# Kernel tuning notes

Hardware: AMD Instinct MI355X
Metric: run time of the kernel (lower is better)

Reference implementation:

```python
import jax, jax.numpy as jnp
import numpy as np

SEQ, B, NIN, NHID = 512, 64, 1024, 1024

def setup_inputs() -> dict:
    key = jax.random.key(0)
    k1, k2, k3 = jax.random.split(key, 3)
    x = jax.random.normal(k1, (SEQ, B, NIN), dtype=jnp.float32)
    # nn.Linear(ninput+nhid, 4*nhid): weight (4*nhid, ninput+nhid), bias (4*nhid,)
    bound = 1.0 / np.sqrt(NIN + NHID)
    W = jax.random.uniform(k2, (4 * NHID, NIN + NHID), dtype=jnp.float32, minval=-bound, maxval=bound)
    b = jax.random.uniform(k3, (4 * NHID,), dtype=jnp.float32, minval=-bound, maxval=bound)
    return {"x": x, "W": W, "b": b}

def reference(x, W, b):
    nhid = W.shape[0] // 4
    batch = x.shape[1]
    # split weight: columns [0:NIN] act on x_t, [NIN:] act on h
    def step(carry, x_t):
        h, c = carry
        a = jnp.concatenate([x_t, h], axis=1) @ W.T + b  # (B, 4*nhid)
        i = jax.nn.sigmoid(a[:, :nhid])
        f = jax.nn.sigmoid(a[:, nhid:2 * nhid])
        o = jax.nn.sigmoid(a[:, 2 * nhid:3 * nhid])
        g = jnp.tanh(a[:, 3 * nhid:])
        c = c * f + i * g
        h = o * jnp.tanh(c)
        return (h, c), h
    h0 = jnp.zeros((batch, nhid), dtype=x.dtype)
    c0 = jnp.zeros((batch, nhid), dtype=x.dtype)
    (h, c), output = jax.lax.scan(step, (h0, c0), x)
    return (output, h)
```

## Files before the change

kernel.cpp:

```cpp
#include <hip/hip_runtime.h>
#include <hip/hip_bf16.h>
#include <stdint.h>
#include <stddef.h>

#define SEQ   512
#define BATCH 64
#define NIN   1024
#define NHID  1024
#define NG    4096

typedef __attribute__((ext_vector_type(8))) short bf16x8;
typedef __attribute__((ext_vector_type(4))) float f32x4;
typedef __attribute__((ext_vector_type(4))) uint32_t u32x4;

static __device__ __forceinline__ ushort f2bf(float f) {
  uint32_t u = __builtin_bit_cast(uint32_t, f);
  uint32_t lsb = (u >> 16) & 1u;
  u += 0x7fffu + lsb;
  return (ushort)(u >> 16);
}
static __device__ __forceinline__ ushort f2h(float f) {
  _Float16 h = (_Float16)f;
  return __builtin_bit_cast(ushort, h);
}
static __device__ __forceinline__ float h2f(ushort u) {
  return (float)__builtin_bit_cast(_Float16, u);
}

static __device__ __forceinline__ f32x4 mfma_bf16(bf16x8 a, bf16x8 b, f32x4 c) {
  return __builtin_amdgcn_mfma_f32_16x16x32_bf16(a, b, c, 0, 0, 0);
}

static __device__ __forceinline__ void lds_load16(const ushort* g, ushort* l) {
  __builtin_amdgcn_global_load_lds(
      (const __attribute__((address_space(1))) void*)g,
      (__attribute__((address_space(3))) void*)l, 16, 0, 0);
}

static __device__ __forceinline__ void st_short_dev(ushort* p, uint32_t v) {
  asm volatile("global_store_short %0, %1, off sc1" :: "v"(p), "v"(v) : "memory");
}
static __device__ __forceinline__ void st_dword_dev(uint32_t* p, uint32_t v) {
  asm volatile("global_store_dword %0, %1, off sc1" :: "v"(p), "v"(v) : "memory");
}
static __device__ __forceinline__ void st_x4_dev(ushort* p, u32x4 v) {
  asm volatile("global_store_dwordx4 %0, %1, off sc1" :: "v"(p), "v"(v) : "memory");
}
static __device__ __forceinline__ uint32_t ld_dword_dev(const uint32_t* p) {
  uint32_t v;
  asm volatile("global_load_dword %0, %1, off sc1" : "=v"(v) : "v"(p) : "memory");
  return v;
}
static __device__ __forceinline__ u32x4 ld_x4_dev(const ushort* p) {
  u32x4 v;
  asm volatile("global_load_dwordx4 %0, %1, off sc1" : "=v"(v) : "v"(p) : "memory");
  return v;
}

#define WAITV(n) do { asm volatile("s_waitcnt vmcnt(" #n ")" ::: "memory"); \
                      __builtin_amdgcn_sched_barrier(0); } while (0)

static __device__ __forceinline__ float sigm_f(float x) {
  return __builtin_amdgcn_rcpf(1.f + __expf(-x));
}
static __device__ __forceinline__ float tanh_f(float x) {
  return 1.f - 2.f * __builtin_amdgcn_rcpf(__expf(2.f * x) + 1.f);
}


__global__ __launch_bounds__(256) void k_convert_x(const float* __restrict__ X,
                                                   ushort* __restrict__ Xb, int n4) {
  int i = blockIdx.x * 256 + threadIdx.x;
  if (i < n4) {
    float4 v = ((const float4*)X)[i];
    ushort4 o;
    o.x = f2bf(v.x); o.y = f2bf(v.y); o.z = f2bf(v.z); o.w = f2bf(v.w);
    ((ushort4*)Xb)[i] = o;
  }
}

__global__ __launch_bounds__(256) void k_convert_w(const float* __restrict__ W,
                                                   const float* __restrict__ bvec,
                                                   ushort* __restrict__ Wxb,
                                                   ushort* __restrict__ Whb,
                                                   float* __restrict__ bp) {
  int p = blockIdx.x;
  int cg = p >> 6, g = (p >> 4) & 3, j = p & 15;
  int r = g * 1024 + cg * 16 + j;
  const float* src = W + (size_t)r * 2048;
  for (int k4 = threadIdx.x; k4 < 512; k4 += 256) {
    float4 v = ((const float4*)src)[k4];
    ushort4 o;
    o.x = f2bf(v.x); o.y = f2bf(v.y); o.z = f2bf(v.z); o.w = f2bf(v.w);
    if (k4 < 256) ((ushort4*)(Wxb + (size_t)p * 1024))[k4] = o;
    else          ((ushort4*)(Whb + (size_t)p * 1024))[k4 - 256] = o;
  }
  if (threadIdx.x == 0) bp[p] = bvec[r];
}

__global__ __launch_bounds__(256) void k_zero(ushort* __restrict__ hb0,
                                              ushort* __restrict__ hb1,
                                              float* __restrict__ cst,
                                              uint32_t* __restrict__ flg2) {
  int i = blockIdx.x * 256 + threadIdx.x;
  st_short_dev(hb0 + i, 0u);
  st_short_dev(hb1 + i, 0u);
  cst[i] = 0.f;
  if (i < 256 * 64) st_dword_dev(flg2 + i, 0u);
}


__global__ __launch_bounds__(256) void k_gemm1(const ushort* __restrict__ Xbc,
                                               const ushort* __restrict__ Wxb,
                                               const float* __restrict__ bp,
                                               ushort* __restrict__ Axc) {
  __shared__ ushort As[128 * 32];
  __shared__ ushort Bs[128 * 32];
  const int m0 = blockIdx.x * 128;
  const int n0 = blockIdx.y * 128;
  const int tid = threadIdx.x;
  const int w = tid >> 6, l = tid & 63;
  const int wr = w >> 1, wc = w & 1;
  const int lr = l >> 2;
  const int lc = (l & 3) * 8;
  const int fr = l & 15, fk8 = (l >> 4) * 8, fq = l >> 4;

  f32x4 acc[4][4] = {};

  for (int kb = 0; kb < 1024; kb += 32) {
    lds_load16(Xbc + (size_t)(m0 + w * 16 + lr) * 1024 + kb + lc,       &As[w * 512]);
    lds_load16(Xbc + (size_t)(m0 + (w + 4) * 16 + lr) * 1024 + kb + lc, &As[(w + 4) * 512]);
    lds_load16(Wxb + (size_t)(n0 + w * 16 + lr) * 1024 + kb + lc,       &Bs[w * 512]);
    lds_load16(Wxb + (size_t)(n0 + (w + 4) * 16 + lr) * 1024 + kb + lc, &Bs[(w + 4) * 512]);
    __syncthreads();
    bf16x8 af[4], bfr[4];
#pragma unroll
    for (int i = 0; i < 4; i++) af[i]  = *(const bf16x8*)&As[(wr * 64 + i * 16 + fr) * 32 + fk8];
#pragma unroll
    for (int i = 0; i < 4; i++) bfr[i] = *(const bf16x8*)&Bs[(wc * 64 + i * 16 + fr) * 32 + fk8];
#pragma unroll
    for (int i = 0; i < 4; i++)
#pragma unroll
      for (int jj = 0; jj < 4; jj++)
        acc[i][jj] = mfma_bf16(af[i], bfr[jj], acc[i][jj]);
    __syncthreads();
  }

#pragma unroll
  for (int jj = 0; jj < 4; jj++) {
    int gc = n0 + wc * 64 + jj * 16 + fr;
    float bb = bp[gc];
#pragma unroll
    for (int i = 0; i < 4; i++) {
      int grb = m0 + wr * 64 + i * 16 + fq * 4;
#pragma unroll
      for (int jr = 0; jr < 4; jr++)
        Axc[(size_t)(grb + jr) * NG + gc] = f2h(acc[i][jj][jr] + bb);
    }
  }
}


__global__ __launch_bounds__(256) void k_persist(const ushort* __restrict__ Whb,
                                                 const ushort* __restrict__ Axc,
                                                 ushort* __restrict__ hb0,
                                                 ushort* __restrict__ hb1,
                                                 float* __restrict__ out,
                                                 uint32_t* __restrict__ flg2,
                                                 float* __restrict__ cst,
                                                 int t0, int TC) {
  __shared__ ushort Wlds[8192 * 8];
  __shared__ float red[4][16][65];
  __shared__ ushort h_sh[16][16];
  __shared__ float houtlds[8][256];

  const int bid = blockIdx.x;
  const int team = bid >> 6, hg = bid & 63;
  const int tid = threadIdx.x, w = tid >> 6, l = tid & 63;
  const int fr = l & 15, fq = l >> 4;

  for (int it = 0; it < 32; ++it) {
    int f = it * 256 + tid;
    int fl = f & 63, bj = (f >> 6) & 3, kc = f >> 8;
    bf16x8 v = *(const bf16x8*)(Whb + (size_t)(hg * 64 + bj * 16 + (fl & 15)) * 1024
                                + kc * 32 + (fl >> 4) * 8);
    *(bf16x8*)&Wlds[(size_t)f * 8] = v;
  }
  __syncthreads();

  const int eb = tid >> 4, ej = tid & 15;
  const int hidx_self = (team * 16 + eb) * 1024 + hg * 16 + ej;
  float creg = cst[hidx_self];

  const size_t roff = (size_t)(team * 16 + fr) * 1024 + w * 256 + fq * 8;
  const uint32_t* fladdr = flg2 + bid * 64 + w * 16 + (l & 15);

  for (int tt = 0; tt < TC; ++tt) {
    const int t = t0 + tt;
    const ushort* hb_r = (t & 1) ? hb0 : hb1;
    ushort*       hb_w = (t & 1) ? hb1 : hb0;

    const ushort* axp = Axc + ((size_t)tt * 64 + team * 16 + eb) * NG + hg * 64;
    ushort axu0 = axp[ej], axu1 = axp[16 + ej], axu2 = axp[32 + ej], axu3 = axp[48 + ej];

    if (t > 0) {
      int guard = 0;
      while (true) {
        uint32_t v0 = ld_dword_dev(fladdr);
        uint32_t v1 = ld_dword_dev(fladdr);
        asm volatile("s_waitcnt vmcnt(1)" ::: "memory");
        __builtin_amdgcn_sched_barrier(0);
        bool ok0 = __all((int)(v0 >= (uint32_t)t));
        asm volatile("s_waitcnt vmcnt(0)" ::: "memory");
        __builtin_amdgcn_sched_barrier(0);
        if (ok0) break;
        if (__all((int)(v1 >= (uint32_t)t))) break;
        if (++guard > (1 << 15)) break;
      }
    }

    const ushort* aBt = hb_r + roff;
    u32x4 hv[8];
    f32x4 acc[4] = {};
#pragma unroll
    for (int ks = 0; ks < 8; ++ks) hv[ks] = ld_x4_dev(aBt + ks * 32);
#define SLICE(ks) do {                                                        \
      bf16x8 a_ = __builtin_bit_cast(bf16x8, hv[ks]);                         \
      _Pragma("unroll")                                                       \
      for (int bj = 0; bj < 4; ++bj) {                                        \
        bf16x8 b_ = *(const bf16x8*)&Wlds[(size_t)(((w * 8 + (ks)) * 4 + bj) * 64 + l) * 8]; \
        acc[bj] = mfma_bf16(a_, b_, acc[bj]);                                 \
      }                                                                       \
    } while (0)
    WAITV(7); SLICE(0);
    WAITV(6); SLICE(1);
    WAITV(5); SLICE(2);
    WAITV(4); SLICE(3);
    WAITV(3); SLICE(4);
    WAITV(2); SLICE(5);
    WAITV(1); SLICE(6);
    WAITV(0); SLICE(7);
#undef SLICE

#pragma unroll
    for (int bj = 0; bj < 4; ++bj)
#pragma unroll
      for (int jr = 0; jr < 4; ++jr)
        red[w][fq * 4 + jr][bj * 16 + fr] = acc[bj][jr];
    __syncthreads();

    float ai_ = h2f(axu0), af_ = h2f(axu1), ao_ = h2f(axu2), ag_ = h2f(axu3);
#pragma unroll
    for (int ww = 0; ww < 4; ++ww) {
      ai_ += red[ww][eb][ej];
      af_ += red[ww][eb][16 + ej];
      ao_ += red[ww][eb][32 + ej];
      ag_ += red[ww][eb][48 + ej];
    }

    float ig = sigm_f(ai_);
    float fg = sigm_f(af_);
    float og = sigm_f(ao_);
    float gg = tanh_f(ag_);
    creg = creg * fg + ig * gg;
    float h = og * tanh_f(creg);
    h_sh[eb][ej] = f2bf(h);
    houtlds[tt & 7][tid] = h;
    __syncthreads();

    if (w == 0) {
      if (l < 32) {
        int prow = l >> 1, phalf = (l & 1) * 8;
        u32x4 pv = *(const u32x4*)&h_sh[prow][phalf];
        st_x4_dev(hb_w + (size_t)(team * 16 + prow) * 1024 + hg * 16 + phalf, pv);
      }
      asm volatile("s_waitcnt vmcnt(0)" ::: "memory");
      __builtin_amdgcn_sched_barrier(0);
      st_dword_dev(flg2 + (team * 64 + l) * 64 + hg, (uint32_t)(t + 1));
    }

    if ((tt & 7) == 7) {
      int tb = t - 7;
#pragma unroll
      for (int s = 0; s < 8; ++s)
        out[(size_t)(tb + s) * 65536 + hidx_self] = houtlds[s][tid];
    }
    if (t == SEQ - 1) out[(size_t)SEQ * 65536 + hidx_self] = h;
  }

  cst[hidx_self] = creg;
}


__global__ __launch_bounds__(256) void k_step(int t,
                                              const ushort* __restrict__ Xb,
                                              const ushort* __restrict__ Wxb,
                                              const ushort* __restrict__ Whb,
                                              const float* __restrict__ bp,
                                              const ushort* __restrict__ hprev,
                                              ushort* __restrict__ hnext,
                                              float* __restrict__ cst,
                                              float* __restrict__ out) {
  __shared__ float red[4][16][65];
  const int bidx = blockIdx.x;
  const int cg = bidx & 63, mb = bidx >> 6;
  const int b0 = mb * 16, pcol = cg * 64;
  const int tid = threadIdx.x, w = tid >> 6, l = tid & 63;
  const int fr = l & 15, fk8 = (l >> 4) * 8, fq = l >> 4;

  f32x4 acc[4] = {};

  const ushort* aSrc;
  const ushort* bMat;
  int kbase;
  if (w < 2) { aSrc = Xb + (size_t)(t * 64 + b0 + fr) * 1024 + w * 512 + fk8; bMat = Wxb; kbase = w * 512; }
  else       { aSrc = hprev + (size_t)(b0 + fr) * 1024 + (w - 2) * 512 + fk8; bMat = Whb; kbase = (w - 2) * 512; }
  const ushort* bRow = bMat + (size_t)(pcol + fr) * 1024 + kbase + fk8;

#pragma unroll
  for (int ks = 0; ks < 16; ks++) {
    int kk = ks * 32;
    bf16x8 a = *(const bf16x8*)(aSrc + kk);
#pragma unroll
    for (int bj = 0; bj < 4; bj++) {
      bf16x8 bfv = *(const bf16x8*)(bRow + (size_t)bj * 16 * 1024 + kk);
      acc[bj] = mfma_bf16(a, bfv, acc[bj]);
    }
  }

#pragma unroll
  for (int bj = 0; bj < 4; bj++)
#pragma unroll
    for (int jr = 0; jr < 4; jr++)
      red[w][fq * 4 + jr][bj * 16 + fr] = acc[bj][jr];
  __syncthreads();

  const int b = tid >> 4, j = tid & 15;
  float ai_ = 0.f, af_ = 0.f, ao_ = 0.f, ag_ = 0.f;
#pragma unroll
  for (int ww = 0; ww < 4; ww++) {
    ai_ += red[ww][b][j];
    af_ += red[ww][b][16 + j];
    ao_ += red[ww][b][32 + j];
    ag_ += red[ww][b][48 + j];
  }
  ai_ += bp[pcol + j]; af_ += bp[pcol + 16 + j]; ao_ += bp[pcol + 32 + j]; ag_ += bp[pcol + 48 + j];

  float ig = sigm_f(ai_);
  float fg = sigm_f(af_);
  float og = sigm_f(ao_);
  float gg = tanh_f(ag_);
  int hidx = (b0 + b) * 1024 + cg * 16 + j;
  float cn = cst[hidx] * fg + ig * gg;
  cst[hidx] = cn;
  float h = og * tanh_f(cn);
  out[(size_t)t * 65536 + hidx] = h;
  hnext[hidx] = f2bf(h);
  if (t == SEQ - 1) out[(size_t)SEQ * 65536 + hidx] = h;
}


extern "C" void kernel_launch(void* const* d_in, const int* in_sizes, int n_in,
                              void* d_out, int out_size, void* d_ws, size_t ws_size,
                              hipStream_t stream) {
  const float* X    = (const float*)d_in[0];
  const float* W    = (const float*)d_in[1];
  const float* bvec = (const float*)d_in[2];
  float* out = (float*)d_out;
  char* ws = (char*)d_ws;

  size_t off = 0;
  auto alloc = [&](size_t bytes) -> char* {
    char* p = ws + off;
    off += (bytes + 255) & ~(size_t)255;
    return p;
  };
  ushort*   Xb   = (ushort*)alloc((size_t)SEQ * BATCH * NIN * 2);
  ushort*   Wxb  = (ushort*)alloc((size_t)NG * NIN * 2);
  ushort*   Whb  = (ushort*)alloc((size_t)NG * NHID * 2);
  float*    bp   = (float*)alloc((size_t)NG * 4);
  ushort*   hb0  = (ushort*)alloc((size_t)BATCH * NHID * 2);
  ushort*   hb1  = (ushort*)alloc((size_t)BATCH * NHID * 2);
  float*    cst  = (float*)alloc((size_t)BATCH * NHID * 4);
  uint32_t* flg2 = (uint32_t*)alloc(256 * 64 * 4);
  size_t base_need = off;

  if (ws_size < base_need) return;

  size_t avail = ws_size - base_need;
  int TC = 0;
  for (int tc = 512; tc >= 16; tc >>= 1) {
    if ((size_t)tc * 64 * NG * 2 <= avail) { TC = tc; break; }
  }
  ushort* Axc = (ushort*)(ws + base_need);

  k_convert_x<<<(SEQ * BATCH * NIN / 4 + 255) / 256, 256, 0, stream>>>(X, Xb, SEQ * BATCH * NIN / 4);
  k_convert_w<<<NG, 256, 0, stream>>>(W, bvec, Wxb, Whb, bp);
  k_zero<<<BATCH * NHID / 256, 256, 0, stream>>>(hb0, hb1, cst, flg2);

  if (TC > 0) {
    for (int c = 0; c < SEQ / TC; ++c) {
      k_gemm1<<<dim3(TC * 64 / 128, NG / 128), 256, 0, stream>>>(
          Xb + (size_t)c * TC * 64 * 1024, Wxb, bp, Axc);
      k_persist<<<256, 256, 0, stream>>>(Whb, Axc, hb0, hb1, out, flg2, cst, c * TC, TC);
    }
  } else {
    for (int t = 0; t < SEQ; t++) {
      const ushort* hp = (t & 1) ? hb1 : hb0;
      ushort*       hn = (t & 1) ? hb0 : hb1;
      k_step<<<256, 256, 0, stream>>>(t, Xb, Wxb, Whb, bp, hp, hn, cst, out);
    }
  }
}
```

Measured before the change: 2.237 ms.

## Overlap input GEMM with recurrence via extra producer warps in persistent kernel

Adds two extra waves per block of the persistent LSTM kernel that compute the next 64-step chunk of the input projection (x·Wx + b) into a double-buffered Axc buffer while the four recurrent waves run the current chunk. Only the first chunk is produced by the standalone GEMM kernel, so the recurrence no longer waits on separate GEMM launches. The intent is to hide the input-GEMM time behind the latency-bound recurrence. The cost is more registers and threads per block, extra memory traffic competing with the critical h exchange, and reliance on barrier ordering between producer and consumer waves for chunk-buffer correctness.

```diff
diff --git a/kernel.cpp b/kernel.cpp
--- a/kernel.cpp
+++ b/kernel.cpp
@@ -54,6 +54,11 @@
 static __device__ __forceinline__ u32x4 ld_x4_dev(const ushort* p) {
   u32x4 v;
   asm volatile("global_load_dwordx4 %0, %1, off sc1" : "=v"(v) : "v"(p) : "memory");
+  return v;
+}
+static __device__ __forceinline__ uint32_t ld_ushort_l2(const ushort* p) {
+  uint32_t v;
+  asm volatile("global_load_ushort %0, %1, off sc0" : "=v"(v) : "v"(p) : "memory");
   return v;
 }
 
@@ -161,14 +166,17 @@
 }
 
 
-__global__ __launch_bounds__(256) void k_persist(const ushort* __restrict__ Whb,
-                                                 const ushort* __restrict__ Axc,
+__global__ __launch_bounds__(384) void k_persist(const ushort* __restrict__ Whb,
+                                                 const ushort* __restrict__ Wxb,
+                                                 const ushort* __restrict__ Xb,
+                                                 const float* __restrict__ bp,
+                                                 ushort* __restrict__ ax0,
+                                                 ushort* __restrict__ ax1,
                                                  ushort* __restrict__ hb0,
                                                  ushort* __restrict__ hb1,
                                                  float* __restrict__ out,
                                                  uint32_t* __restrict__ flg2,
-                                                 float* __restrict__ cst,
-                                                 int t0, int TC) {
+                                                 float* __restrict__ cst) {
   __shared__ ushort Wlds[8192 * 8];
   __shared__ float red[4][16][65];
   __shared__ ushort h_sh[16][16];
@@ -179,51 +187,60 @@
   const int tid = threadIdx.x, w = tid >> 6, l = tid & 63;
   const int fr = l & 15, fq = l >> 4;
 
-  for (int it = 0; it < 32; ++it) {
-    int f = it * 256 + tid;
-    int fl = f & 63, bj = (f >> 6) & 3, kc = f >> 8;
+  for (int it = tid; it < 8192; it += 384) {
+    int fl = it & 63, bj = (it >> 6) & 3, kc = it >> 8;
     bf16x8 v = *(const bf16x8*)(Whb + (size_t)(hg * 64 + bj * 16 + (fl & 15)) * 1024
                                 + kc * 32 + (fl >> 4) * 8);
-    *(bf16x8*)&Wlds[(size_t)f * 8] = v;
+    *(bf16x8*)&Wlds[(size_t)it * 8] = v;
   }
   __syncthreads();
 
   const int eb = tid >> 4, ej = tid & 15;
-  const int hidx_self = (team * 16 + eb) * 1024 + hg * 16 + ej;
-  float creg = cst[hidx_self];
+  const int hidx_self = (team * 16 + (eb & 15)) * 1024 + hg * 16 + ej;
+  float creg = (w < 4) ? cst[hidx_self] : 0.f;
 
   const size_t roff = (size_t)(team * 16 + fr) * 1024 + w * 256 + fq * 8;
   const uint32_t* fladdr = flg2 + bid * 64 + w * 16 + (l & 15);
 
-  for (int tt = 0; tt < TC; ++tt) {
-    const int t = t0 + tt;
-    const ushort* hb_r = (t & 1) ? hb0 : hb1;
-    ushort*       hb_w = (t & 1) ? hb1 : hb0;
-
-    const ushort* axp = Axc + ((size_t)tt * 64 + team * 16 + eb) * NG + hg * 64;
-    ushort axu0 = axp[ej], axu1 = axp[16 + ej], axu2 = axp[32 + ej], axu3 = axp[48 + ej];
-
-    if (t > 0) {
-      int guard = 0;
-      while (true) {
-        uint32_t v0 = ld_dword_dev(fladdr);
-        uint32_t v1 = ld_dword_dev(fladdr);
-        asm volatile("s_waitcnt vmcnt(1)" ::: "memory");
-        __builtin_amdgcn_sched_barrier(0);
-        bool ok0 = __all((int)(v0 >= (uint32_t)t));
-        asm volatile("s_waitcnt vmcnt(0)" ::: "memory");
-        __builtin_amdgcn_sched_barrier(0);
-        if (ok0) break;
-        if (__all((int)(v1 >= (uint32_t)t))) break;
-        if (++guard > (1 << 15)) break;
+  const int wg = w - 4;
+  const float bb0 = bp[hg * 64 + (wg & 1) * 32 + fr];
+  const float bb1 = bp[hg * 64 + (wg & 1) * 32 + 16 + fr];
+
+  for (int tt = 0; tt < SEQ; ++tt) {
+    const int c = tt >> 6, tl = tt & 63;
+    const ushort* Axc = (c & 1) ? ax1 : ax0;
+    ushort*       Axn = (c & 1) ? ax0 : ax1;
+    const ushort* hb_r = (tt & 1) ? hb0 : hb1;
+    ushort*       hb_w = (tt & 1) ? hb1 : hb0;
+
+    if (w < 4) {
+      const ushort* axp = Axc + ((size_t)tl * 64 + team * 16 + eb) * NG + hg * 64;
+      ushort axu0 = (ushort)ld_ushort_l2(axp + ej);
+      ushort axu1 = (ushort)ld_ushort_l2(axp + 16 + ej);
+      ushort axu2 = (ushort)ld_ushort_l2(axp + 32 + ej);
+      ushort axu3 = (ushort)ld_ushort_l2(axp + 48 + ej);
+
+      if (tt > 0) {
+        int guard = 0;
+        while (true) {
+          uint32_t v0 = ld_dword_dev(fladdr);
+          uint32_t v1 = ld_dword_dev(fladdr);
+          asm volatile("s_waitcnt vmcnt(1)" ::: "memory");
+          __builtin_amdgcn_sched_barrier(0);
+          bool ok0 = __all((int)(v0 >= (uint32_t)tt));
+          asm volatile("s_waitcnt vmcnt(0)" ::: "memory");
+          __builtin_amdgcn_sched_barrier(0);
+          if (ok0) break;
+          if (__all((int)(v1 >= (uint32_t)tt))) break;
+          if (++guard > (1 << 15)) break;
+        }
       }
-    }
-
-    const ushort* aBt = hb_r + roff;
-    u32x4 hv[8];
-    f32x4 acc[4] = {};
-#pragma unroll
-    for (int ks = 0; ks < 8; ++ks) hv[ks] = ld_x4_dev(aBt + ks * 32);
+
+      const ushort* aBt = hb_r + roff;
+      u32x4 hv[8];
+      f32x4 acc[4] = {};
+#pragma unroll
+      for (int ks = 0; ks < 8; ++ks) hv[ks] = ld_x4_dev(aBt + ks * 32);
 #define SLICE(ks) do {                                                        \
       bf16x8 a_ = __builtin_bit_cast(bf16x8, hv[ks]);                         \
       _Pragma("unroll")                                                       \
@@ -232,63 +249,92 @@
         acc[bj] = mfma_bf16(a_, b_, acc[bj]);                                 \
       }                                                                       \
     } while (0)
-    WAITV(7); SLICE(0);
-    WAITV(6); SLICE(1);
-    WAITV(5); SLICE(2);
-    WAITV(4); SLICE(3);
-    WAITV(3); SLICE(4);
-    WAITV(2); SLICE(5);
-    WAITV(1); SLICE(6);
-    WAITV(0); SLICE(7);
+      WAITV(7); SLICE(0);
+      WAITV(6); SLICE(1);
+      WAITV(5); SLICE(2);
+      WAITV(4); SLICE(3);
+      WAITV(3); SLICE(4);
+      WAITV(2); SLICE(5);
+      WAITV(1); SLICE(6);
+      WAITV(0); SLICE(7);
 #undef SLICE
 
 #pragma unroll
-    for (int bj = 0; bj < 4; ++bj)
-#pragma unroll
-      for (int jr = 0; jr < 4; ++jr)
-        red[w][fq * 4 + jr][bj * 16 + fr] = acc[bj][jr];
-    __syncthreads();
-
-    float ai_ = h2f(axu0), af_ = h2f(axu1), ao_ = h2f(axu2), ag_ = h2f(axu3);
-#pragma unroll
-    for (int ww = 0; ww < 4; ++ww) {
-      ai_ += red[ww][eb][ej];
-      af_ += red[ww][eb][16 + ej];
-      ao_ += red[ww][eb][32 + ej];
-      ag_ += red[ww][eb][48 + ej];
+      for (int bj = 0; bj < 4; ++bj)
+#pragma unroll
+        for (int jr = 0; jr < 4; ++jr)
+          red[w][fq * 4 + jr][bj * 16 + fr] = acc[bj][jr];
+
+      red[w][fq * 4][64] = 0.f;
+      __syncthreads();
+
+      float ai_ = h2f(axu0), af_ = h2f(axu1), ao_ = h2f(axu2), ag_ = h2f(axu3);
+#pragma unroll
+      for (int ww = 0; ww < 4; ++ww) {
+        ai_ += red[ww][eb][ej];
+        af_ += red[ww][eb][16 + ej];
+        ao_ += red[ww][eb][32 + ej];
+        ag_ += red[ww][eb][48 + ej];
+      }
+
+      float ig = sigm_f(ai_);
+      float fg = sigm_f(af_);
+      float og = sigm_f(ao_);
+      float gg = tanh_f(ag_);
+      creg = creg * fg + ig * gg;
+      float h = og * tanh_f(creg);
+      h_sh[eb][ej] = f2bf(h);
+      houtlds[tt & 7][tid] = h;
+      __syncthreads();
+
+      if (w == 0) {
+        if (l < 32) {
+          int prow = l >> 1, phalf = (l & 1) * 8;
+          u32x4 pv = *(const u32x4*)&h_sh[prow][phalf];
+          st_x4_dev(hb_w + (size_t)(team * 16 + prow) * 1024 + hg * 16 + phalf, pv);
+        }
+        asm volatile("s_waitcnt vmcnt(0)" ::: "memory");
+        __builtin_amdgcn_sched_barrier(0);
+        st_dword_dev(flg2 + (team * 64 + l) * 64 + hg, (uint32_t)(tt + 1));
+      }
+
+      if ((tt & 7) == 7) {
+        int tb = tt - 7;
+#pragma unroll
+        for (int s = 0; s < 8; ++s)
+          out[(size_t)(tb + s) * 65536 + hidx_self] = houtlds[s][tid];
+      }
+      if (tt == SEQ - 1) out[(size_t)SEQ * 65536 + hidx_self] = h;
+
+    } else {
+      if (c + 1 < 8) {
+        int sg = (c + 1) * 64 + tl;
+        const ushort* ax_ = Xb + ((size_t)sg * 64 + team * 16 + fr) * 1024 + fq * 8;
+        const ushort* bx_ = Wxb + (size_t)(hg * 64 + wg * 32 + fr) * 1024 + fq * 8;
+        f32x4 g0 = {}, g1 = {};
+#pragma unroll 4
+        for (int ks = 0; ks < 32; ++ks) {
+          bf16x8 a_ = *(const bf16x8*)(ax_ + ks * 32);
+          bf16x8 b0 = *(const bf16x8*)(bx_ + ks * 32);
+          bf16x8 b1 = *(const bf16x8*)(bx_ + (size_t)16 * 1024 + ks * 32);
+          g0 = mfma_bf16(a_, b0, g0);
+          g1 = mfma_bf16(a_, b1, g1);
+        }
+#pragma unroll
+        for (int jr = 0; jr < 4; ++jr) {
+          ushort* axo = Axn + ((size_t)tl * 64 + team * 16 + fq * 4 + jr) * NG
+                        + hg * 64 + wg * 32 + fr;
+          axo[0]  = f2h(g0[jr] + bb0);
+          axo[16] = f2h(g1[jr] + bb1);
+        }
+        asm volatile("s_waitcnt vmcnt(0)" ::: "memory");
+      }
+      __syncthreads();
+      __syncthreads();
     }
-
-    float ig = sigm_f(ai_);
-    float fg = sigm_f(af_);
-    float og = sigm_f(ao_);
-    float gg = tanh_f(ag_);
-    creg = creg * fg + ig * gg;
-    float h = og * tanh_f(creg);
-    h_sh[eb][ej] = f2bf(h);
-    houtlds[tt & 7][tid] = h;
-    __syncthreads();
-
-    if (w == 0) {
-      if (l < 32) {
-        int prow = l >> 1, phalf = (l & 1) * 8;
-        u32x4 pv = *(const u32x4*)&h_sh[prow][phalf];
-        st_x4_dev(hb_w + (size_t)(team * 16 + prow) * 1024 + hg * 16 + phalf, pv);
-      }
-      asm volatile("s_waitcnt vmcnt(0)" ::: "memory");
-      __builtin_amdgcn_sched_barrier(0);
-      st_dword_dev(flg2 + (team * 64 + l) * 64 + hg, (uint32_t)(t + 1));
-    }
-
-    if ((tt & 7) == 7) {
-      int tb = t - 7;
-#pragma unroll
-      for (int s = 0; s < 8; ++s)
-        out[(size_t)(tb + s) * 65536 + hidx_self] = houtlds[s][tid];
-    }
-    if (t == SEQ - 1) out[(size_t)SEQ * 65536 + hidx_self] = h;
-  }
-
-  cst[hidx_self] = creg;
+  }
+
+  if (w < 4) cst[hidx_self] = creg;
 }
 
 
@@ -384,26 +430,21 @@
   float*    cst  = (float*)alloc((size_t)BATCH * NHID * 4);
   uint32_t* flg2 = (uint32_t*)alloc(256 * 64 * 4);
   size_t base_need = off;
+  ushort*   ax0  = (ushort*)alloc((size_t)64 * BATCH * NG * 2);
+  ushort*   ax1  = (ushort*)alloc((size_t)64 * BATCH * NG * 2);
+  size_t fused_need = off;
 
   if (ws_size < base_need) return;
-
-  size_t avail = ws_size - base_need;
-  int TC = 0;
-  for (int tc = 512; tc >= 16; tc >>= 1) {
-    if ((size_t)tc * 64 * NG * 2 <= avail) { TC = tc; break; }
-  }
-  ushort* Axc = (ushort*)(ws + base_need);
+  const bool fused = (ws_size >= fused_need);
 
   k_convert_x<<<(SEQ * BATCH * NIN / 4 + 255) / 256, 256, 0, stream>>>(X, Xb, SEQ * BATCH * NIN / 4);
   k_convert_w<<<NG, 256, 0, stream>>>(W, bvec, Wxb, Whb, bp);
   k_zero<<<BATCH * NHID / 256, 256, 0, stream>>>(hb0, hb1, cst, flg2);
 
-  if (TC > 0) {
-    for (int c = 0; c < SEQ / TC; ++c) {
-      k_gemm1<<<dim3(TC * 64 / 128, NG / 128), 256, 0, stream>>>(
-          Xb + (size_t)c * TC * 64 * 1024, Wxb, bp, Axc);
-      k_persist<<<256, 256, 0, stream>>>(Whb, Axc, hb0, hb1, out, flg2, cst, c * TC, TC);
-    }
+  if (fused) {
+    k_gemm1<<<dim3(32, 32), 256, 0, stream>>>(Xb, Wxb, bp, ax0);
+    k_persist<<<256, 384, 0, stream>>>(Whb, Wxb, Xb, bp, ax0, ax1,
+                                       hb0, hb1, out, flg2, cst);
   } else {
     for (int t = 0; t < SEQ; t++) {
       const ushort* hp = (t & 1) ? hb1 : hb0;
```

After: 4.282 ms. +91.4%, slower.

## Add 256x256-tile 8-wave input-projection GEMM with async LDS double buffering

Applied to the files above, without the earlier changes.

Adds a new input-projection GEMM kernel that runs when the whole sequence fits in workspace. It uses 256x256 tiles with 8 waves, XOR-swizzled LDS, direct global-to-LDS loads double-buffered and interleaved with MFMA phases, s_setprio around the MFMAs, and a block-ID remap for L2 locality. The goal is higher MFMA throughput and more operand reuse than the old 128x128 kernel, cutting the precompute portion of the runtime. It uses one block per CU with a large LDS footprint and depends on the workspace being big enough for TC=512.

```diff
diff --git a/kernel.cpp b/kernel.cpp
--- a/kernel.cpp
+++ b/kernel.cpp
@@ -107,6 +107,99 @@
   st_short_dev(hb1 + i, 0u);
   cst[i] = 0.f;
   if (i < 256 * 64) st_dword_dev(flg2 + i, 0u);
+}
+
+
+#define G8_PHASE(MS, NS, STAGE) do {                                          \
+    __syncthreads();                                                          \
+    STAGE;                                                                    \
+    bf16x8 aF[4][2], bF[2][2];                                                \
+    _Pragma("unroll") for (int mf = 0; mf < 4; ++mf) {                        \
+      int R = wr * 128 + (MS) * 64 + mf * 16 + fr;                            \
+      _Pragma("unroll") for (int kk = 0; kk < 2; ++kk)                        \
+        aF[mf][kk] = *(const bf16x8*)&lds[bufc * 32768 + R * 64 +             \
+                       ((kk * 32 + fq * 8) ^ ((fr & 7) << 3))];               \
+    }                                                                         \
+    _Pragma("unroll") for (int nf = 0; nf < 2; ++nf) {                        \
+      int R = wc * 64 + (NS) * 32 + nf * 16 + fr;                             \
+      _Pragma("unroll") for (int kk = 0; kk < 2; ++kk)                        \
+        bF[nf][kk] = *(const bf16x8*)&lds[bufc * 32768 + 16384 + R * 64 +     \
+                       ((kk * 32 + fq * 8) ^ ((fr & 7) << 3))];               \
+    }                                                                         \
+    __builtin_amdgcn_s_setprio(1);                                            \
+    _Pragma("unroll") for (int mf = 0; mf < 4; ++mf)                          \
+      _Pragma("unroll") for (int nf = 0; nf < 2; ++nf)                        \
+        _Pragma("unroll") for (int kk = 0; kk < 2; ++kk)                      \
+          acc[(MS) * 4 + mf][(NS) * 2 + nf] =                                 \
+            mfma_bf16(aF[mf][kk], bF[nf][kk], acc[(MS)*4+mf][(NS)*2+nf]);     \
+    __builtin_amdgcn_s_setprio(0);                                            \
+  } while (0)
+
+__global__ __launch_bounds__(512, 1) void k_gemm8(const ushort* __restrict__ Xbc,
+                                                  const ushort* __restrict__ Wxb,
+                                                  const float* __restrict__ bp,
+                                                  ushort* __restrict__ Axc) {
+  __shared__ ushort lds[65536];
+
+  const int tid = threadIdx.x;
+  const int w = tid >> 6, l = tid & 63;
+  const int wr = w >> 2, wc = w & 3;
+  const int fr = l & 15, fq = l >> 4;
+  const int lrow = l >> 3;
+  const int jsw = (l & 7) ^ lrow;
+
+  int raw = blockIdx.x;
+  int id = (raw & 7) * 256 + (raw >> 3);
+  const int m0 = (id >> 4) * 256;
+  const int n0 = (id & 15) * 256;
+
+  auto stageA = [&](int buf, int H, int kt) {
+    if (kt > 15) return;
+    int R0a = w * 8 + H * 64;
+    int R0b = 128 + w * 8 + H * 64;
+    lds_load16(Xbc + (size_t)(m0 + R0a + lrow) * 1024 + kt * 64 + jsw * 8,
+               &lds[buf * 32768 + R0a * 64]);
+    lds_load16(Xbc + (size_t)(m0 + R0b + lrow) * 1024 + kt * 64 + jsw * 8,
+               &lds[buf * 32768 + R0b * 64]);
+  };
+  auto stageB = [&](int buf, int H, int kt) {
+    if (kt > 15) return;
+    int R0a = (w >> 2) * 64 + (w & 3) * 8 + H * 32;
+    int R0b = R0a + 128;
+    lds_load16(Wxb + (size_t)(n0 + R0a + lrow) * 1024 + kt * 64 + jsw * 8,
+               &lds[buf * 32768 + 16384 + R0a * 64]);
+    lds_load16(Wxb + (size_t)(n0 + R0b + lrow) * 1024 + kt * 64 + jsw * 8,
+               &lds[buf * 32768 + 16384 + R0b * 64]);
+  };
+
+  f32x4 acc[8][4] = {};
+
+  stageA(0, 0, 0); stageB(0, 0, 0); stageB(0, 1, 0); stageA(0, 1, 0);
+  stageA(1, 0, 1); stageB(1, 0, 1);
+
+  for (int j = 0; j < 16; ++j) {
+    const int bufc = j & 1, bufn = bufc ^ 1;
+    if (j < 15) { WAITV(4); } else { WAITV(0); }
+    G8_PHASE(0, 0, stageB(bufn, 1, j + 1));
+    G8_PHASE(0, 1, stageA(bufn, 1, j + 1));
+    G8_PHASE(1, 0, stageA(bufc, 0, j + 2));
+    G8_PHASE(1, 1, stageB(bufc, 0, j + 2));
+  }
+
+  float bias_[4];
+#pragma unroll
+  for (int nf = 0; nf < 4; ++nf) bias_[nf] = bp[n0 + wc * 64 + nf * 16 + fr];
+#pragma unroll
+  for (int mf = 0; mf < 8; ++mf) {
+    int rowb = m0 + wr * 128 + mf * 16 + fq * 4;
+#pragma unroll
+    for (int nf = 0; nf < 4; ++nf) {
+      int col = n0 + wc * 64 + nf * 16 + fr;
+#pragma unroll
+      for (int jr = 0; jr < 4; ++jr)
+        Axc[(size_t)(rowb + jr) * NG + col] = f2h(acc[mf][nf][jr] + bias_[nf]);
+    }
+  }
 }
 
 
@@ -398,7 +491,10 @@
   k_convert_w<<<NG, 256, 0, stream>>>(W, bvec, Wxb, Whb, bp);
   k_zero<<<BATCH * NHID / 256, 256, 0, stream>>>(hb0, hb1, cst, flg2);
 
-  if (TC > 0) {
+  if (TC == 512) {
+    k_gemm8<<<2048, 512, 0, stream>>>(Xb, Wxb, bp, Axc);
+    k_persist<<<256, 256, 0, stream>>>(Whb, Axc, hb0, hb1, out, flg2, cst, 0, 512);
+  } else if (TC > 0) {
     for (int c = 0; c < SEQ / TC; ++c) {
       k_gemm1<<<dim3(TC * 64 / 128, NG / 128), 256, 0, stream>>>(
           Xb + (size_t)c * TC * 64 * 1024, Wxb, bp, Axc);
```

New measurement: 2.223 ms. Within noise of the previous version (-0.6%).
